# Kernel tuning notes

Measured on AMD Instinct MI355X. Metric: run time of the kernel, lower is better.

Reference implementation:

```python
import jax, jax.numpy as jnp
import numpy as np

N_DIALOGS = 60
DIA_LEN = 100
N = N_DIALOGS * DIA_LEN  # 6000 utterances total
D_IN = 512
D_OUT = 512


def setup_inputs() -> dict:
    key = jax.random.key(0)
    k1, k2, k3, k4 = jax.random.split(key, 4)
    inputs = jax.random.normal(k1, (N, D_IN), dtype=jnp.float32)
    # per-dialog lengths (concrete host array; defines static graph structure)
    dia_len = np.full((N_DIALOGS,), DIA_LEN, dtype=np.int64)
    # one-hot speaker mask [N, 1, 2]; qmask[j,0,0]==1 -> speaker0 else speaker1
    sp = jax.random.randint(k2, (N,), 0, 2)
    qmask = jnp.zeros((N, 1, 2), jnp.int64).at[jnp.arange(N), 0, sp].set(1)
    W = jax.random.normal(k3, (D_OUT, D_IN), dtype=jnp.float32) / np.sqrt(D_IN)
    b = jax.random.normal(k4, (D_OUT,), dtype=jnp.float32) * 0.01
    return {"inputs": inputs, "dia_len": dia_len, "qmask": qmask, "W": W, "b": b}


def build_adj(inputs, dia_len, qmask):
    # Vectorized equivalent of message_passing_directed_speaker:
    # adj = I; edge (i,j) iff i,j in same dialog, same speaker, and consecutive
    # among that speaker's utterances; weight = 1 - arccos(clip(cos,-1,1))/pi.
    n = inputs.shape[0]
    dia_len_np = np.asarray(dia_len)
    did = jnp.asarray(np.repeat(np.arange(len(dia_len_np)), dia_len_np))  # dialog id per node
    sp0 = qmask[:, 0, 0] == 1  # True -> speaker0
    cs0 = jnp.cumsum(sp0.astype(jnp.int32))
    cs1 = jnp.cumsum((~sp0).astype(jnp.int32))
    csel = jnp.where(sp0, cs0, cs1)  # running count of own speaker
    idx = jnp.arange(n)
    # j>i, same dialog, same speaker, no same-speaker utterance strictly between
    upper = ((did[None, :] == did[:, None])
             & (sp0[None, :] == sp0[:, None])
             & (csel[None, :] - csel[:, None] == 1)
             & (idx[None, :] > idx[:, None]))
    edge = upper | upper.T
    # pairwise cosine similarity (cossim returns 0 when a norm is 0)
    nrm = jnp.sqrt(jnp.sum(inputs * inputs, axis=-1))  # [N]
    denom = nrm[:, None] * nrm[None, :]
    dots = inputs @ inputs.T  # [N, N]
    cos = jnp.where(denom > 0, dots / jnp.where(denom > 0, denom, 1.0), 0.0)
    cos_safe = jnp.where(edge, jnp.clip(cos, -1.0, 1.0), 0.0)
    w = 1.0 - jnp.arccos(cos_safe) / jnp.pi
    return jnp.where(edge, w, 0.0) + jnp.eye(n, dtype=inputs.dtype)


def reference(inputs, dia_len, qmask, W, b):
    adj = build_adj(inputs, dia_len, qmask)  # [N, N]
    x = adj @ inputs                          # [N, D_IN]
    return x @ W.T + b                        # [N, D_OUT]
```

## Files before the change

kernel.cpp:

```cpp
#include <hip/hip_runtime.h>
#include <hip/hip_bf16.h>

#define N_NODES 6000
#define DIA     100
#define DDIM    512
#define NPAD    6016

typedef short short8   __attribute__((ext_vector_type(8)));
typedef float floatx4  __attribute__((ext_vector_type(4)));

__device__ __forceinline__ unsigned short f2bf(float f) {
    unsigned int u = __float_as_uint(f);
    unsigned int r = (u + 0x7fffu + ((u >> 16) & 1u)) >> 16;
    return (unsigned short)r;
}

__device__ __forceinline__ float wave_reduce_sum(float v) {
    #pragma unroll
    for (int off = 32; off > 0; off >>= 1) v += __shfl_xor(v, off, 64);
    return v;
}

__global__ __launch_bounds__(256) void prep_kernel(
    const float* __restrict__ x, const int* __restrict__ qmask,
    const float* __restrict__ W, float* __restrict__ nrm2,
    int* __restrict__ nxt, int* __restrict__ prv, unsigned short* __restrict__ wbf)
{
    int bid = blockIdx.x;
    int tid = threadIdx.x;
    if (bid < N_NODES / 4) {
        int wv = tid >> 6, lane = tid & 63;
        int i = bid * 4 + wv;
        const float* row = x + (size_t)i * DDIM;
        float4 a = *(const float4*)(row + lane * 8);
        float4 b = *(const float4*)(row + lane * 8 + 4);
        float s = a.x*a.x + a.y*a.y + a.z*a.z + a.w*a.w
                + b.x*b.x + b.y*b.y + b.z*b.z + b.w*b.w;
        s = wave_reduce_sum(s);

        int sp = qmask[2 * i];
        int dstart = (i / DIA) * DIA;
        int dend   = dstart + DIA;

        int cand = i + 1 + lane;
        unsigned long long b1 = __ballot((cand < dend) && (qmask[2 * cand] == sp));
        int nx = -1;
        if (b1) {
            nx = i + __ffsll(b1);
        } else {
            int cand2 = i + 65 + lane;
            unsigned long long b2 =
                __ballot((lane < 35) && (cand2 < dend) && (qmask[2 * cand2] == sp));
            if (b2) nx = i + 64 + __ffsll(b2);
        }
        int candp = i - 1 - lane;
        unsigned long long p1 = __ballot((candp >= dstart) && (qmask[2 * candp] == sp));
        int pv = -1;
        if (p1) {
            pv = i - __ffsll(p1);
        } else {
            int candp2 = i - 65 - lane;
            unsigned long long p2 =
                __ballot((lane < 35) && (candp2 >= dstart) && (qmask[2 * candp2] == sp));
            if (p2) pv = i - 64 - __ffsll(p2);
        }
        if (lane == 0) { nrm2[i] = s; nxt[i] = nx; prv[i] = pv; }
    } else {
        int base = (bid - N_NODES / 4) * 2048 + tid * 8;
        float4 a = *(const float4*)(W + base);
        float4 b = *(const float4*)(W + base + 4);
        union { unsigned short u[8]; short8 v; } o;
        o.u[0]=f2bf(a.x); o.u[1]=f2bf(a.y); o.u[2]=f2bf(a.z); o.u[3]=f2bf(a.w);
        o.u[4]=f2bf(b.x); o.u[5]=f2bf(b.y); o.u[6]=f2bf(b.z); o.u[7]=f2bf(b.w);
        *(short8*)(wbf + base) = o.v;
    }
}

__global__ __launch_bounds__(256) void edge_kernel(
    const float* __restrict__ x, const float* __restrict__ nrm2,
    const int* __restrict__ nxt, float* __restrict__ wn)
{
    int wv = threadIdx.x >> 6, lane = threadIdx.x & 63;
    int i = blockIdx.x * 4 + wv;
    int j = nxt[i];
    if (j < 0) { if (lane == 0) wn[i] = 0.0f; return; }
    const float* ri = x + (size_t)i * DDIM;
    const float* rj = x + (size_t)j * DDIM;
    float4 a0 = *(const float4*)(ri + lane * 8);
    float4 a1 = *(const float4*)(ri + lane * 8 + 4);
    float4 b0 = *(const float4*)(rj + lane * 8);
    float4 b1 = *(const float4*)(rj + lane * 8 + 4);
    float d = a0.x*b0.x + a0.y*b0.y + a0.z*b0.z + a0.w*b0.w
            + a1.x*b1.x + a1.y*b1.y + a1.z*b1.z + a1.w*b1.w;
    d = wave_reduce_sum(d);
    if (lane == 0) {
        float dn = nrm2[i] * nrm2[j];
        float c = (dn > 0.0f) ? (d / sqrtf(dn)) : 0.0f;
        c = fminf(1.0f, fmaxf(-1.0f, c));
        wn[i] = 1.0f - acosf(c) * 0.3183098861837907f;
    }
}

__global__ __launch_bounds__(256) void build_kernel(
    const float* __restrict__ x, const int* __restrict__ nxt,
    const int* __restrict__ prv, const float* __restrict__ wn,
    unsigned short* __restrict__ xbf)
{
    int wv = threadIdx.x >> 6, lane = threadIdx.x & 63;
    int i = blockIdx.x * 4 + wv;
    unsigned short* orow = xbf + (size_t)i * DDIM + lane * 8;
    if (i >= N_NODES) {
        short8 z = (short8)0;
        *(short8*)orow = z;
        return;
    }
    const float* ri = x + (size_t)i * DDIM + lane * 8;
    float acc[8];
    {
        float4 a = *(const float4*)(ri);
        float4 b = *(const float4*)(ri + 4);
        acc[0]=a.x; acc[1]=a.y; acc[2]=a.z; acc[3]=a.w;
        acc[4]=b.x; acc[5]=b.y; acc[6]=b.z; acc[7]=b.w;
    }
    int j = nxt[i];
    if (j >= 0) {
        float w = wn[i];
        const float* rj = x + (size_t)j * DDIM + lane * 8;
        float4 a = *(const float4*)(rj);
        float4 b = *(const float4*)(rj + 4);
        acc[0]+=w*a.x; acc[1]+=w*a.y; acc[2]+=w*a.z; acc[3]+=w*a.w;
        acc[4]+=w*b.x; acc[5]+=w*b.y; acc[6]+=w*b.z; acc[7]+=w*b.w;
    }
    int p = prv[i];
    if (p >= 0) {
        float w = wn[p];
        const float* rp = x + (size_t)p * DDIM + lane * 8;
        float4 a = *(const float4*)(rp);
        float4 b = *(const float4*)(rp + 4);
        acc[0]+=w*a.x; acc[1]+=w*a.y; acc[2]+=w*a.z; acc[3]+=w*a.w;
        acc[4]+=w*b.x; acc[5]+=w*b.y; acc[6]+=w*b.z; acc[7]+=w*b.w;
    }
    union { unsigned short u[8]; short8 v; } o;
    #pragma unroll
    for (int t = 0; t < 8; ++t) o.u[t] = f2bf(acc[t]);
    *(short8*)orow = o.v;
}

__global__ __launch_bounds__(256) void gemm_kernel(
    const unsigned short* __restrict__ xbf, const unsigned short* __restrict__ wbf,
    const float* __restrict__ bias, float* __restrict__ out)
{
    int wave = threadIdx.x >> 6, lane = threadIdx.x & 63;
    int m0 = blockIdx.x * 64 + (wave & 1) * 32;
    int n0 = blockIdx.y * 64 + (wave >> 1) * 32;
    int fr = lane & 15;
    int kq = (lane >> 4) * 8;

    floatx4 acc[2][2] = {};
    const unsigned short* ab = xbf + (size_t)(m0 + fr) * DDIM + kq;
    const unsigned short* bb = wbf + (size_t)(n0 + fr) * DDIM + kq;

    #pragma unroll 4
    for (int k = 0; k < DDIM; k += 32) {
        short8 a0 = *(const short8*)(ab + k);
        short8 a1 = *(const short8*)(ab + 16 * DDIM + k);
        short8 b0 = *(const short8*)(bb + k);
        short8 b1 = *(const short8*)(bb + 16 * DDIM + k);
        acc[0][0] = __builtin_amdgcn_mfma_f32_16x16x32_bf16(a0, b0, acc[0][0], 0, 0, 0);
        acc[0][1] = __builtin_amdgcn_mfma_f32_16x16x32_bf16(a0, b1, acc[0][1], 0, 0, 0);
        acc[1][0] = __builtin_amdgcn_mfma_f32_16x16x32_bf16(a1, b0, acc[1][0], 0, 0, 0);
        acc[1][1] = __builtin_amdgcn_mfma_f32_16x16x32_bf16(a1, b1, acc[1][1], 0, 0, 0);
    }

    int col = lane & 15;
    int rbase = (lane >> 4) * 4;
    #pragma unroll
    for (int ms = 0; ms < 2; ++ms) {
        #pragma unroll
        for (int ns = 0; ns < 2; ++ns) {
            int n = n0 + ns * 16 + col;
            float bv = bias[n];
            #pragma unroll
            for (int r = 0; r < 4; ++r) {
                int m = m0 + ms * 16 + rbase + r;
                if (m < N_NODES)
                    out[(size_t)m * DDIM + n] = acc[ms][ns][r] + bv;
            }
        }
    }
}

extern "C" void kernel_launch(void* const* d_in, const int* in_sizes, int n_in,
                              void* d_out, int out_size, void* d_ws, size_t ws_size,
                              hipStream_t stream) {
    const float* inputs = (const float*)d_in[0];
    const int* qmask   = (const int*)d_in[2];
    const float* W     = (const float*)d_in[3];
    const float* bias  = (const float*)d_in[4];
    float* out = (float*)d_out;

    char* ws = (char*)d_ws;
    unsigned short* xbf = (unsigned short*)ws;
    unsigned short* wbf = xbf + (size_t)NPAD * DDIM;
    float* nrm2 = (float*)(wbf + (size_t)DDIM * DDIM);
    int*   nxt  = (int*)(nrm2 + N_NODES);
    int*   prv  = (int*)(nxt + N_NODES);
    float* wn   = (float*)(prv + N_NODES);

    prep_kernel <<<dim3(N_NODES / 4 + 128), 256, 0, stream>>>(inputs, qmask, W, nrm2, nxt, prv, wbf);
    edge_kernel <<<dim3(N_NODES / 4),       256, 0, stream>>>(inputs, nrm2, nxt, wn);
    build_kernel<<<dim3(NPAD / 4),          256, 0, stream>>>(inputs, nxt, prv, wn, xbf);
    gemm_kernel <<<dim3(94, 8),             256, 0, stream>>>(xbf, wbf, bias, out);
}
```

Before: 106.4 us.

## Fuse prep, edge and build kernels into one per-dialog block kernel

Replaces the three preprocessing launches with a single kernel where each 1024-thread block handles one whole dialog, keeping norms, speaker ids, neighbour links and edge weights in shared memory and separating phases with block barriers. Neighbour search becomes a simple serial scan over the 100-entry speaker array in LDS. This removes two kernel launches and the global round-trips for intermediates, but only 60 blocks do the row work, so most of the GPU's compute units sit idle during that phase.

```diff
diff --git a/kernel.cpp b/kernel.cpp
--- a/kernel.cpp
+++ b/kernel.cpp
@@ -2,6 +2,7 @@
 #include <hip/hip_bf16.h>
 
 #define N_NODES 6000
+#define N_DIA   60
 #define DIA     100
 #define DDIM    512
 #define NPAD    6016
@@ -21,129 +22,116 @@
     return v;
 }
 
-__global__ __launch_bounds__(256) void prep_kernel(
+__global__ __launch_bounds__(1024) void fused_prep(
     const float* __restrict__ x, const int* __restrict__ qmask,
-    const float* __restrict__ W, float* __restrict__ nrm2,
-    int* __restrict__ nxt, int* __restrict__ prv, unsigned short* __restrict__ wbf)
+    const float* __restrict__ W, unsigned short* __restrict__ xbf,
+    unsigned short* __restrict__ wbf)
 {
     int bid = blockIdx.x;
     int tid = threadIdx.x;
-    if (bid < N_NODES / 4) {
-        int wv = tid >> 6, lane = tid & 63;
-        int i = bid * 4 + wv;
-        const float* row = x + (size_t)i * DDIM;
-        float4 a = *(const float4*)(row + lane * 8);
-        float4 b = *(const float4*)(row + lane * 8 + 4);
-        float s = a.x*a.x + a.y*a.y + a.z*a.z + a.w*a.w
-                + b.x*b.x + b.y*b.y + b.z*b.z + b.w*b.w;
-        s = wave_reduce_sum(s);
-
-        int sp = qmask[2 * i];
-        int dstart = (i / DIA) * DIA;
-        int dend   = dstart + DIA;
-
-        int cand = i + 1 + lane;
-        unsigned long long b1 = __ballot((cand < dend) && (qmask[2 * cand] == sp));
-        int nx = -1;
-        if (b1) {
-            nx = i + __ffsll(b1);
-        } else {
-            int cand2 = i + 65 + lane;
-            unsigned long long b2 =
-                __ballot((lane < 35) && (cand2 < dend) && (qmask[2 * cand2] == sp));
-            if (b2) nx = i + 64 + __ffsll(b2);
-        }
-        int candp = i - 1 - lane;
-        unsigned long long p1 = __ballot((candp >= dstart) && (qmask[2 * candp] == sp));
-        int pv = -1;
-        if (p1) {
-            pv = i - __ffsll(p1);
-        } else {
-            int candp2 = i - 65 - lane;
-            unsigned long long p2 =
-                __ballot((lane < 35) && (candp2 >= dstart) && (qmask[2 * candp2] == sp));
-            if (p2) pv = i - 64 - __ffsll(p2);
-        }
-        if (lane == 0) { nrm2[i] = s; nxt[i] = nx; prv[i] = pv; }
-    } else {
-        int base = (bid - N_NODES / 4) * 2048 + tid * 8;
+    if (bid >= N_DIA) {
+        int base = (bid - N_DIA) * 8192 + tid * 8;
         float4 a = *(const float4*)(W + base);
         float4 b = *(const float4*)(W + base + 4);
         union { unsigned short u[8]; short8 v; } o;
         o.u[0]=f2bf(a.x); o.u[1]=f2bf(a.y); o.u[2]=f2bf(a.z); o.u[3]=f2bf(a.w);
         o.u[4]=f2bf(b.x); o.u[5]=f2bf(b.y); o.u[6]=f2bf(b.z); o.u[7]=f2bf(b.w);
         *(short8*)(wbf + base) = o.v;
-    }
-}
-
-__global__ __launch_bounds__(256) void edge_kernel(
-    const float* __restrict__ x, const float* __restrict__ nrm2,
-    const int* __restrict__ nxt, float* __restrict__ wn)
-{
-    int wv = threadIdx.x >> 6, lane = threadIdx.x & 63;
-    int i = blockIdx.x * 4 + wv;
-    int j = nxt[i];
-    if (j < 0) { if (lane == 0) wn[i] = 0.0f; return; }
-    const float* ri = x + (size_t)i * DDIM;
-    const float* rj = x + (size_t)j * DDIM;
-    float4 a0 = *(const float4*)(ri + lane * 8);
-    float4 a1 = *(const float4*)(ri + lane * 8 + 4);
-    float4 b0 = *(const float4*)(rj + lane * 8);
-    float4 b1 = *(const float4*)(rj + lane * 8 + 4);
-    float d = a0.x*b0.x + a0.y*b0.y + a0.z*b0.z + a0.w*b0.w
-            + a1.x*b1.x + a1.y*b1.y + a1.z*b1.z + a1.w*b1.w;
-    d = wave_reduce_sum(d);
-    if (lane == 0) {
-        float dn = nrm2[i] * nrm2[j];
-        float c = (dn > 0.0f) ? (d / sqrtf(dn)) : 0.0f;
-        c = fminf(1.0f, fmaxf(-1.0f, c));
-        wn[i] = 1.0f - acosf(c) * 0.3183098861837907f;
-    }
-}
-
-__global__ __launch_bounds__(256) void build_kernel(
-    const float* __restrict__ x, const int* __restrict__ nxt,
-    const int* __restrict__ prv, const float* __restrict__ wn,
-    unsigned short* __restrict__ xbf)
-{
-    int wv = threadIdx.x >> 6, lane = threadIdx.x & 63;
-    int i = blockIdx.x * 4 + wv;
-    unsigned short* orow = xbf + (size_t)i * DDIM + lane * 8;
-    if (i >= N_NODES) {
-        short8 z = (short8)0;
-        *(short8*)orow = z;
+        if (bid == N_DIA) {
+            short8 z = (short8)0;
+            *(short8*)(xbf + (size_t)N_NODES * DDIM + tid * 8) = z;
+        }
         return;
     }
-    const float* ri = x + (size_t)i * DDIM + lane * 8;
-    float acc[8];
-    {
-        float4 a = *(const float4*)(ri);
-        float4 b = *(const float4*)(ri + 4);
-        acc[0]=a.x; acc[1]=a.y; acc[2]=a.z; acc[3]=a.w;
-        acc[4]=b.x; acc[5]=b.y; acc[6]=b.z; acc[7]=b.w;
+
+    __shared__ float nrm2_s[DIA];
+    __shared__ float wn_s[DIA];
+    __shared__ int   sp_s[DIA];
+    __shared__ int   nxt_s[DIA];
+    __shared__ int   prv_s[DIA];
+
+    int nbase = bid * DIA;
+    int wv = tid >> 6, lane = tid & 63;
+
+    if (tid < DIA) sp_s[tid] = qmask[2 * (nbase + tid)];
+    __syncthreads();
+
+    if (tid < DIA) {
+        int sp = sp_s[tid];
+        int nx = -1;
+        for (int j = tid + 1; j < DIA; ++j) if (sp_s[j] == sp) { nx = j; break; }
+        int pv = -1;
+        for (int j = tid - 1; j >= 0; --j) if (sp_s[j] == sp) { pv = j; break; }
+        nxt_s[tid] = nx; prv_s[tid] = pv;
     }
-    int j = nxt[i];
-    if (j >= 0) {
-        float w = wn[i];
-        const float* rj = x + (size_t)j * DDIM + lane * 8;
-        float4 a = *(const float4*)(rj);
-        float4 b = *(const float4*)(rj + 4);
-        acc[0]+=w*a.x; acc[1]+=w*a.y; acc[2]+=w*a.z; acc[3]+=w*a.w;
-        acc[4]+=w*b.x; acc[5]+=w*b.y; acc[6]+=w*b.z; acc[7]+=w*b.w;
+
+    for (int r = wv; r < DIA; r += 16) {
+        const float* row = x + (size_t)(nbase + r) * DDIM + lane * 8;
+        float4 a = *(const float4*)(row);
+        float4 b = *(const float4*)(row + 4);
+        float s = a.x*a.x + a.y*a.y + a.z*a.z + a.w*a.w
+                + b.x*b.x + b.y*b.y + b.z*b.z + b.w*b.w;
+        s = wave_reduce_sum(s);
+        if (lane == 0) nrm2_s[r] = s;
     }
-    int p = prv[i];
-    if (p >= 0) {
-        float w = wn[p];
-        const float* rp = x + (size_t)p * DDIM + lane * 8;
-        float4 a = *(const float4*)(rp);
-        float4 b = *(const float4*)(rp + 4);
-        acc[0]+=w*a.x; acc[1]+=w*a.y; acc[2]+=w*a.z; acc[3]+=w*a.w;
-        acc[4]+=w*b.x; acc[5]+=w*b.y; acc[6]+=w*b.z; acc[7]+=w*b.w;
+    __syncthreads();
+
+    for (int r = wv; r < DIA; r += 16) {
+        int j = nxt_s[r];
+        if (j >= 0) {
+            const float* ri = x + (size_t)(nbase + r) * DDIM + lane * 8;
+            const float* rj = x + (size_t)(nbase + j) * DDIM + lane * 8;
+            float4 a0 = *(const float4*)(ri);
+            float4 a1 = *(const float4*)(ri + 4);
+            float4 b0 = *(const float4*)(rj);
+            float4 b1 = *(const float4*)(rj + 4);
+            float d = a0.x*b0.x + a0.y*b0.y + a0.z*b0.z + a0.w*b0.w
+                    + a1.x*b1.x + a1.y*b1.y + a1.z*b1.z + a1.w*b1.w;
+            d = wave_reduce_sum(d);
+            if (lane == 0) {
+                float dn = nrm2_s[r] * nrm2_s[j];
+                float c = (dn > 0.0f) ? (d / sqrtf(dn)) : 0.0f;
+                c = fminf(1.0f, fmaxf(-1.0f, c));
+                wn_s[r] = 1.0f - acosf(c) * 0.3183098861837907f;
+            }
+        } else if (lane == 0) {
+            wn_s[r] = 0.0f;
+        }
     }
-    union { unsigned short u[8]; short8 v; } o;
-    #pragma unroll
-    for (int t = 0; t < 8; ++t) o.u[t] = f2bf(acc[t]);
-    *(short8*)orow = o.v;
+    __syncthreads();
+
+    for (int r = wv; r < DIA; r += 16) {
+        const float* ri = x + (size_t)(nbase + r) * DDIM + lane * 8;
+        float acc[8];
+        {
+            float4 a = *(const float4*)(ri);
+            float4 b = *(const float4*)(ri + 4);
+            acc[0]=a.x; acc[1]=a.y; acc[2]=a.z; acc[3]=a.w;
+            acc[4]=b.x; acc[5]=b.y; acc[6]=b.z; acc[7]=b.w;
+        }
+        int j = nxt_s[r];
+        if (j >= 0) {
+            float w = wn_s[r];
+            const float* rj = x + (size_t)(nbase + j) * DDIM + lane * 8;
+            float4 a = *(const float4*)(rj);
+            float4 b = *(const float4*)(rj + 4);
+            acc[0]+=w*a.x; acc[1]+=w*a.y; acc[2]+=w*a.z; acc[3]+=w*a.w;
+            acc[4]+=w*b.x; acc[5]+=w*b.y; acc[6]+=w*b.z; acc[7]+=w*b.w;
+        }
+        int p = prv_s[r];
+        if (p >= 0) {
+            float w = wn_s[p];
+            const float* rp = x + (size_t)(nbase + p) * DDIM + lane * 8;
+            float4 a = *(const float4*)(rp);
+            float4 b = *(const float4*)(rp + 4);
+            acc[0]+=w*a.x; acc[1]+=w*a.y; acc[2]+=w*a.z; acc[3]+=w*a.w;
+            acc[4]+=w*b.x; acc[5]+=w*b.y; acc[6]+=w*b.z; acc[7]+=w*b.w;
+        }
+        union { unsigned short u[8]; short8 v; } o;
+        #pragma unroll
+        for (int t = 0; t < 8; ++t) o.u[t] = f2bf(acc[t]);
+        *(short8*)(xbf + (size_t)(nbase + r) * DDIM + lane * 8) = o.v;
+    }
 }
 
 __global__ __launch_bounds__(256) void gemm_kernel(
@@ -202,13 +190,7 @@
     char* ws = (char*)d_ws;
     unsigned short* xbf = (unsigned short*)ws;
     unsigned short* wbf = xbf + (size_t)NPAD * DDIM;
-    float* nrm2 = (float*)(wbf + (size_t)DDIM * DDIM);
-    int*   nxt  = (int*)(nrm2 + N_NODES);
-    int*   prv  = (int*)(nxt + N_NODES);
-    float* wn   = (float*)(prv + N_NODES);
 
-    prep_kernel <<<dim3(N_NODES / 4 + 128), 256, 0, stream>>>(inputs, qmask, W, nrm2, nxt, prv, wbf);
-    edge_kernel <<<dim3(N_NODES / 4),       256, 0, stream>>>(inputs, nrm2, nxt, wn);
-    build_kernel<<<dim3(NPAD / 4),          256, 0, stream>>>(inputs, nxt, prv, wn, xbf);
-    gemm_kernel <<<dim3(94, 8),             256, 0, stream>>>(xbf, wbf, bias, out);
+    fused_prep <<<dim3(N_DIA + 32), 1024, 0, stream>>>(inputs, qmask, W, xbf, wbf);
+    gemm_kernel<<<dim3(94, 8),      256,  0, stream>>>(xbf, wbf, bias, out);
 }
```

New measurement: 111.2 us. 4.6% more time.
